# Optimization experiments

Hardware: AMD Instinct MI355X
Metric: run time of the kernel (lower is better)

The kernel has to match this reference:

```python
import jax, jax.numpy as jnp
import numpy as np

C_S = 128
C_T = 128
C_OUT = 128


def _proj(x, W, b):
    # 1x1x1 Conv3d == per-voxel linear over channel dim. x: [B, Cin, T, H, W]
    return jnp.einsum('oc,bcthw->bothw', W, x) + b[None, :, None, None, None]


def setup_inputs() -> dict:
    key = jax.random.key(0)
    ks = jax.random.split(key, 12)
    B, T, H, W = 4, 4, 32, 32
    spatial_features = jax.random.normal(ks[0], (B, T, C_S, H, W), dtype=jnp.float32)
    temporal_features = jax.random.normal(ks[1], (B, C_T, T, H, W), dtype=jnp.float32)
    def w(k, o, i):
        return jax.random.normal(k, (o, i), dtype=jnp.float32) * (i ** -0.5)
    return {
        'spatial_features': spatial_features,
        'temporal_features': temporal_features,
        'Wq': w(ks[2], C_OUT, C_S), 'bq': jnp.zeros((C_OUT,), jnp.float32),
        'Wk': w(ks[3], C_OUT, C_T), 'bk': jnp.zeros((C_OUT,), jnp.float32),
        'Wv': w(ks[4], C_OUT, C_T), 'bv': jnp.zeros((C_OUT,), jnp.float32),
        'Wo': w(ks[5], C_OUT, C_OUT), 'bo': jnp.zeros((C_OUT,), jnp.float32),
    }


def reference(spatial_features, temporal_features, Wq, bq, Wk, bk, Wv, bv, Wo, bo):
    B, T, C_s, H, W = spatial_features.shape
    N = T * H * W
    scale = C_OUT ** -0.5
    # permute(0,2,1,3,4): [B, T, C_s, H, W] -> [B, C_s, T, H, W]
    x_s = jnp.transpose(spatial_features, (0, 2, 1, 3, 4))
    q = _proj(x_s, Wq, bq)                 # [B, C_out, T, H, W]
    k = _proj(temporal_features, Wk, bk)   # [B, C_out, T, H, W]
    v = _proj(temporal_features, Wv, bv)   # [B, C_out, T, H, W]
    Q = q.reshape(B, C_OUT, N).transpose(0, 2, 1)  # [B, N, C]
    K = k.reshape(B, C_OUT, N)                     # [B, C, N]
    V = v.reshape(B, C_OUT, N).transpose(0, 2, 1)  # [B, N, C]
    attn = jax.nn.softmax(jnp.einsum('bnc,bcm->bnm', Q, K) * scale, axis=2)  # [B, N, N]
    out = jnp.einsum('bnm,bmc->bnc', attn, V)      # [B, N, C]
    out = out.transpose(0, 2, 1).reshape(B, C_OUT, T, H, W)
    return _proj(out, Wo, bo)
```

## Files before the change

### kernel.cpp

```cpp
#include <hip/hip_runtime.h>
#include <cstddef>

#define NDIM 4096
#define SCALE 0.08838834764831843f
#define SOFT_BIAS 8.0f

typedef _Float16 h8 __attribute__((ext_vector_type(8)));
typedef _Float16 h4 __attribute__((ext_vector_type(4)));
typedef _Float16 h2 __attribute__((ext_vector_type(2)));
typedef float    f4 __attribute__((ext_vector_type(4)));

__global__ __launch_bounds__(256) void prep_w_kernel(
    const float* __restrict__ Wq, const float* __restrict__ Wk,
    const float* __restrict__ Wv, const float* __restrict__ Wo,
    _Float16* __restrict__ Wh)
{
    const int idx = (blockIdx.x * 256 + threadIdx.x) * 8;
    const int sel = idx >> 14;
    const float* src = sel == 0 ? Wq : sel == 1 ? Wk : sel == 2 ? Wv : Wo;
    const int off = idx & 16383;
    const float4 a = *(const float4*)(src + off);
    const float4 c = *(const float4*)(src + off + 4);
    h8 r;
    r[0]=(_Float16)a.x; r[1]=(_Float16)a.y; r[2]=(_Float16)a.z; r[3]=(_Float16)a.w;
    r[4]=(_Float16)c.x; r[5]=(_Float16)c.y; r[6]=(_Float16)c.z; r[7]=(_Float16)c.w;
    *(h8*)(Wh + idx) = r;
}

__global__ __launch_bounds__(64) void proj_q_kernel(
    const float* __restrict__ spatial, const _Float16* __restrict__ Whq,
    const float* __restrict__ bq, _Float16* __restrict__ Qh)
{
    __shared__ __align__(16) _Float16 Xl[16 * 136];
    const int lane = threadIdx.x;
    const int n0   = blockIdx.x * 16;
    const int b    = blockIdx.y;
    const int t    = n0 >> 10, hw0 = n0 & 1023;
    const int n16  = lane & 15, q4 = lane >> 4;

    {
        const float* sb = spatial + (((size_t)(b * 4 + t) * 128 + q4 * 32) << 10) + hw0 + n16;
        #pragma unroll
        for (int cp = 0; cp < 16; ++cp) {
            const float v0 = sb[(size_t)(2 * cp) << 10];
            const float v1 = sb[(size_t)(2 * cp + 1) << 10];
            h2 pk; pk[0] = (_Float16)v0; pk[1] = (_Float16)v1;
            *(h2*)&Xl[n16 * 136 + q4 * 32 + 2 * cp] = pk;
        }
    }
    __builtin_amdgcn_wave_barrier();

    h8 xf[4];
    #pragma unroll
    for (int ks = 0; ks < 4; ++ks)
        xf[ks] = *(const h8*)&Xl[n16 * 136 + 32 * ks + 8 * q4];

    f4 acc[8];
    #pragma unroll
    for (int ot = 0; ot < 8; ++ot) acc[ot] = (f4)0.0f;

    #pragma unroll
    for (int ot = 0; ot < 8; ++ot)
        #pragma unroll
        for (int ks = 0; ks < 4; ++ks) {
            const h8 af = *(const h8*)(Whq + (16 * ot + n16) * 128 + 32 * ks + 8 * q4);
            acc[ot] = __builtin_amdgcn_mfma_f32_16x16x32_f16(af, xf[ks], acc[ot], 0, 0, 0);
        }

    #pragma unroll
    for (int ot = 0; ot < 8; ++ot) {
        const float4 bb = *(const float4*)&bq[16 * ot + 4 * q4];
        h4 r;
        r[0]=(_Float16)(acc[ot][0]+bb.x); r[1]=(_Float16)(acc[ot][1]+bb.y);
        r[2]=(_Float16)(acc[ot][2]+bb.z); r[3]=(_Float16)(acc[ot][3]+bb.w);
        *(h4*)(Qh + ((size_t)b * NDIM + n0 + n16) * 128 + 16 * ot + 4 * q4) = r;
    }
}

__global__ __launch_bounds__(64) void proj_kv_kernel(
    const float* __restrict__ temporal, const _Float16* __restrict__ Whk,
    const _Float16* __restrict__ Whv, const float* __restrict__ bk,
    const float* __restrict__ bv, _Float16* __restrict__ Kh, _Float16* __restrict__ Vt)
{
    __shared__ __align__(16) _Float16 Xl[16 * 136];
    const int lane = threadIdx.x;
    const int n0   = blockIdx.x * 16;
    const int b    = blockIdx.y;
    const int n16  = lane & 15, q4 = lane >> 4;

    {
        const float* sb = temporal + (((size_t)(b * 128 + q4 * 32)) << 12) + n0 + n16;
        #pragma unroll
        for (int cp = 0; cp < 16; ++cp) {
            const float v0 = sb[(size_t)(2 * cp) << 12];
            const float v1 = sb[(size_t)(2 * cp + 1) << 12];
            h2 pk; pk[0] = (_Float16)v0; pk[1] = (_Float16)v1;
            *(h2*)&Xl[n16 * 136 + q4 * 32 + 2 * cp] = pk;
        }
    }
    __builtin_amdgcn_wave_barrier();

    h8 xf[4];
    #pragma unroll
    for (int ks = 0; ks < 4; ++ks)
        xf[ks] = *(const h8*)&Xl[n16 * 136 + 32 * ks + 8 * q4];

    f4 accK[8], accV[8];
    #pragma unroll
    for (int i = 0; i < 8; ++i) { accK[i] = (f4)0.0f; accV[i] = (f4)0.0f; }

    #pragma unroll
    for (int ot = 0; ot < 8; ++ot)
        #pragma unroll
        for (int ks = 0; ks < 4; ++ks) {
            const h8 af = *(const h8*)(Whk + (16 * ot + n16) * 128 + 32 * ks + 8 * q4);
            accK[ot] = __builtin_amdgcn_mfma_f32_16x16x32_f16(af, xf[ks], accK[ot], 0, 0, 0);
        }
    #pragma unroll
    for (int ct = 0; ct < 8; ++ct)
        #pragma unroll
        for (int ks = 0; ks < 4; ++ks) {
            const h8 bf = *(const h8*)(Whv + (16 * ct + n16) * 128 + 32 * ks + 8 * q4);
            accV[ct] = __builtin_amdgcn_mfma_f32_16x16x32_f16(xf[ks], bf, accV[ct], 0, 0, 0);
        }

    #pragma unroll
    for (int ot = 0; ot < 8; ++ot) {
        const float4 bb = *(const float4*)&bk[16 * ot + 4 * q4];
        h4 r;
        r[0]=(_Float16)(accK[ot][0]+bb.x); r[1]=(_Float16)(accK[ot][1]+bb.y);
        r[2]=(_Float16)(accK[ot][2]+bb.z); r[3]=(_Float16)(accK[ot][3]+bb.w);
        *(h4*)(Kh + ((size_t)b * NDIM + n0 + n16) * 128 + 16 * ot + 4 * q4) = r;
    }
    #pragma unroll
    for (int ct = 0; ct < 8; ++ct) {
        const float bb = bv[16 * ct + n16];
        h4 r;
        r[0]=(_Float16)(accV[ct][0]+bb); r[1]=(_Float16)(accV[ct][1]+bb);
        r[2]=(_Float16)(accV[ct][2]+bb); r[3]=(_Float16)(accV[ct][3]+bb);
        *(h4*)(Vt + ((size_t)(b * 128 + 16 * ct + n16) << 12) + n0 + 4 * q4) = r;
    }
}

__global__ __launch_bounds__(512, 2) void attn_kernel(
    const _Float16* __restrict__ Qh, const _Float16* __restrict__ Kh,
    const _Float16* __restrict__ Vt, _Float16* __restrict__ Opart,
    float* __restrict__ lpart)
{
    __shared__ __align__(16) _Float16 sh[19712];
    _Float16* __restrict__ Kt = sh;
    _Float16* __restrict__ Vl = sh + 4352;
    _Float16* __restrict__ Pa = sh + 9472;

    const int tid  = threadIdx.x;
    const int w    = tid >> 6, lane = tid & 63;
    const int g    = w >> 1,  p    = w & 1;
    const int n16  = lane & 15, q4 = lane >> 4;
    const int b    = blockIdx.z, hf = blockIdx.y;
    const int n0   = blockIdx.x * 256;
    const int mb   = hf * 1024;

    _Float16* __restrict__ Pg = Pa + g * (64 * 40);

    h8 qf[2][4];
    {
        const _Float16* Qb = Qh + ((size_t)b * NDIM + n0 + 64 * g + 32 * p + n16) * 128;
        #pragma unroll
        for (int qs = 0; qs < 2; ++qs)
            #pragma unroll
            for (int ks = 0; ks < 4; ++ks)
                qf[qs][ks] = *(const h8*)(Qb + (size_t)(16 * qs) * 128 + 32 * ks + 8 * q4);
    }

    const int km  = tid >> 4, kc8 = (tid & 15) * 8;
    const int vc  = tid >> 2, vm8 = (tid & 3) * 8;
    const _Float16* kp = Kh + ((size_t)b * NDIM + mb + km) * 128 + kc8;
    const _Float16* vp = Vt + (((size_t)(b * 128 + vc)) << 12) + mb + vm8;
    int4 kreg = *(const int4*)kp;
    int4 vreg = *(const int4*)vp;

    f4 oacc[4][4];
    #pragma unroll
    for (int i = 0; i < 4; ++i)
        #pragma unroll
        for (int j = 0; j < 4; ++j) oacc[i][j] = (f4)0.0f;
    float lsum[2] = {0.0f, 0.0f};

    for (int it = 0; it < 32; ++it) {
        __syncthreads();
        *(int4*)&Kt[km * 136 + kc8] = kreg;
        *(int4*)&Vl[vc * 40  + vm8] = vreg;
        __syncthreads();

        if (it < 31) {
            kp += 32 * 128; vp += 32;
            kreg = *(const int4*)kp;
            vreg = *(const int4*)vp;
        }

        f4 sacc[2][2];
        #pragma unroll
        for (int mt = 0; mt < 2; ++mt) { sacc[mt][0] = (f4)0.0f; sacc[mt][1] = (f4)0.0f; }
        #pragma unroll
        for (int mt = 0; mt < 2; ++mt)
            #pragma unroll
            for (int ks = 0; ks < 4; ++ks) {
                const h8 kf = *(const h8*)&Kt[(16 * mt + n16) * 136 + 32 * ks + 8 * q4];
                sacc[mt][0] = __builtin_amdgcn_mfma_f32_16x16x32_f16(kf, qf[0][ks], sacc[mt][0], 0, 0, 0);
                sacc[mt][1] = __builtin_amdgcn_mfma_f32_16x16x32_f16(kf, qf[1][ks], sacc[mt][1], 0, 0, 0);
            }

        #pragma unroll
        for (int mt = 0; mt < 2; ++mt)
            #pragma unroll
            for (int qs = 0; qs < 2; ++qs) {
                h4 pk;
                #pragma unroll
                for (int r = 0; r < 4; ++r) {
                    const float e = __expf(fmaf(sacc[mt][qs][r], SCALE, -SOFT_BIAS));
                    lsum[qs] += e;
                    pk[r] = (_Float16)e;
                }
                *(h4*)&Pg[(32 * p + 16 * qs + n16) * 40 + 16 * mt + 4 * q4] = pk;
            }
        __syncthreads();

        h8 pf[4], vf[4];
        #pragma unroll
        for (int qs4 = 0; qs4 < 4; ++qs4)
            pf[qs4] = *(const h8*)&Pg[(16 * qs4 + n16) * 40 + 8 * q4];
        #pragma unroll
        for (int ct = 0; ct < 4; ++ct)
            vf[ct] = *(const h8*)&Vl[(64 * p + 16 * ct + n16) * 40 + 8 * q4];
        #pragma unroll
        for (int qs4 = 0; qs4 < 4; ++qs4)
            #pragma unroll
            for (int ct = 0; ct < 4; ++ct)
                oacc[qs4][ct] = __builtin_amdgcn_mfma_f32_16x16x32_f16(pf[qs4], vf[ct], oacc[qs4][ct], 0, 0, 0);
    }

    #pragma unroll
    for (int qs = 0; qs < 2; ++qs) {
        lsum[qs] += __shfl_xor(lsum[qs], 16, 64);
        lsum[qs] += __shfl_xor(lsum[qs], 32, 64);
    }
    if (lane < 16) {
        float* lb = lpart + (size_t)(hf * 4 + b) * NDIM + n0 + 64 * g + 32 * p;
        lb[lane]      = lsum[0];
        lb[16 + lane] = lsum[1];
    }

    for (int g2 = 0; g2 < 4; ++g2) {
        __syncthreads();
        if (g == g2) {
            #pragma unroll
            for (int qs4 = 0; qs4 < 4; ++qs4)
                #pragma unroll
                for (int ct = 0; ct < 4; ++ct)
                    #pragma unroll
                    for (int r = 0; r < 4; ++r)
                        sh[(16 * qs4 + 4 * q4 + r) * 136 + 64 * p + 16 * ct + n16] =
                            (_Float16)oacc[qs4][ct][r];
        }
        __syncthreads();
        const size_t ob = ((size_t)(hf * 4 + b) * NDIM + n0 + 64 * g2) * 128;
        #pragma unroll
        for (int i = 0; i < 2; ++i) {
            const int ii  = tid + 512 * i;
            const int row = ii >> 4, c8 = (ii & 15) * 8;
            *(int4*)(Opart + ob + (size_t)row * 128 + c8) = *(const int4*)&sh[row * 136 + c8];
        }
    }
}

__global__ __launch_bounds__(64) void proj_final_kernel(
    const _Float16* __restrict__ Opart, const float* __restrict__ lpart,
    const _Float16* __restrict__ Who, const float* __restrict__ bo,
    float* __restrict__ out)
{
    __shared__ __align__(16) _Float16 Xl[16 * 136];
    const int lane = threadIdx.x;
    const int n0   = blockIdx.x * 16;
    const int b    = blockIdx.y;
    const int n16  = lane & 15, q4 = lane >> 4;

    #pragma unroll
    for (int i = 0; i < 4; ++i) {
        const int ii  = lane + 64 * i;
        const int row = ii >> 4, c8 = (ii & 15) * 8;
        float vals[8] = {0,0,0,0,0,0,0,0};
        float l = 0.0f;
        #pragma unroll
        for (int hf = 0; hf < 4; ++hf) {
            const size_t base = ((size_t)(hf * 4 + b) * NDIM + n0 + row) * 128 + c8;
            const h8 o = *(const h8*)(Opart + base);
            #pragma unroll
            for (int j = 0; j < 8; ++j) vals[j] += (float)o[j];
            l += lpart[(size_t)(hf * 4 + b) * NDIM + n0 + row];
        }
        const float rinv = 1.0f / l;
        h8 r;
        #pragma unroll
        for (int j = 0; j < 8; ++j) r[j] = (_Float16)(vals[j] * rinv);
        *(h8*)&Xl[row * 136 + c8] = r;
    }
    __builtin_amdgcn_wave_barrier();

    h8 xf[4];
    #pragma unroll
    for (int ks = 0; ks < 4; ++ks)
        xf[ks] = *(const h8*)&Xl[n16 * 136 + 32 * ks + 8 * q4];

    f4 acc[8];
    #pragma unroll
    for (int ot = 0; ot < 8; ++ot) acc[ot] = (f4)0.0f;

    #pragma unroll
    for (int ot = 0; ot < 8; ++ot)
        #pragma unroll
        for (int ks = 0; ks < 4; ++ks) {
            const h8 af = *(const h8*)(Who + (16 * ot + n16) * 128 + 32 * ks + 8 * q4);
            acc[ot] = __builtin_amdgcn_mfma_f32_16x16x32_f16(af, xf[ks], acc[ot], 0, 0, 0);
        }

    #pragma unroll
    for (int ot = 0; ot < 8; ++ot) {
        const float4 bb = *(const float4*)&bo[16 * ot + 4 * q4];
        const float bias[4] = {bb.x, bb.y, bb.z, bb.w};
        #pragma unroll
        for (int r = 0; r < 4; ++r)
            out[((size_t)(b * 128 + 16 * ot + 4 * q4 + r) << 12) + n0 + n16] =
                acc[ot][r] + bias[r];
    }
}

extern "C" void kernel_launch(void* const* d_in, const int* in_sizes, int n_in,
                              void* d_out, int out_size, void* d_ws, size_t ws_size,
                              hipStream_t stream)
{
    const float* spatial  = (const float*)d_in[0];
    const float* temporal = (const float*)d_in[1];
    const float* Wq = (const float*)d_in[2];
    const float* bq = (const float*)d_in[3];
    const float* Wk = (const float*)d_in[4];
    const float* bk = (const float*)d_in[5];
    const float* Wv = (const float*)d_in[6];
    const float* bv = (const float*)d_in[7];
    const float* Wo = (const float*)d_in[8];
    const float* bo = (const float*)d_in[9];

    char* ws = (char*)d_ws;
    _Float16* Qh    = (_Float16*)(ws);
    _Float16* Kh    = (_Float16*)(ws + (4u  << 20));
    _Float16* Vt    = (_Float16*)(ws + (8u  << 20));
    _Float16* Opart = (_Float16*)(ws + (12u << 20));
    float*    lpart = (float*)   (ws + (28u << 20));
    _Float16* Wh    = (_Float16*)(ws + (28u << 20) + (256u << 10));

    prep_w_kernel<<<32, 256, 0, stream>>>(Wq, Wk, Wv, Wo, Wh);
    proj_q_kernel<<<dim3(256, 4), 64, 0, stream>>>(spatial, Wh, bq, Qh);
    proj_kv_kernel<<<dim3(256, 4), 64, 0, stream>>>(temporal, Wh + 16384, Wh + 32768,
                                                    bk, bv, Kh, Vt);
    attn_kernel<<<dim3(16, 4, 4), 512, 0, stream>>>(Qh, Kh, Vt, Opart, lpart);
    proj_final_kernel<<<dim3(256, 4), 64, 0, stream>>>(Opart, lpart, Wh + 49152, bo,
                                                       (float*)d_out);
}
```

Measured before the change: 157.9 us.

## Fuse Q/K/V projections, retile attention to 256 threads, coalesce I/O

```diff
diff --git a/kernel.cpp b/kernel.cpp
--- a/kernel.cpp
+++ b/kernel.cpp
@@ -27,127 +27,125 @@
     *(h8*)(Wh + idx) = r;
 }
 
-__global__ __launch_bounds__(64) void proj_q_kernel(
-    const float* __restrict__ spatial, const _Float16* __restrict__ Whq,
-    const float* __restrict__ bq, _Float16* __restrict__ Qh)
+__global__ __launch_bounds__(256, 1) void proj_qkv_kernel(
+    const float* __restrict__ spatial, const float* __restrict__ temporal,
+    const _Float16* __restrict__ Wh,
+    const float* __restrict__ bq, const float* __restrict__ bk,
+    const float* __restrict__ bv,
+    _Float16* __restrict__ Qh, _Float16* __restrict__ Kh, _Float16* __restrict__ Vt)
 {
-    __shared__ __align__(16) _Float16 Xl[16 * 136];
-    const int lane = threadIdx.x;
-    const int n0   = blockIdx.x * 16;
-    const int b    = blockIdx.y;
-    const int t    = n0 >> 10, hw0 = n0 & 1023;
-    const int n16  = lane & 15, q4 = lane >> 4;
+    __shared__ __align__(16) _Float16 Xs[64 * 152];
+    __shared__ __align__(16) _Float16 Xt[64 * 152];
+    const int tid = threadIdx.x;
+    const int n0  = blockIdx.x * 64;
+    const int b   = blockIdx.y;
+    const int t   = n0 >> 10, hw0 = n0 & 1023;
+
+    #pragma unroll
+    for (int i = 0; i < 8; ++i) {
+        const int ii = tid + 256 * i;
+        const int c = ii >> 4, j = ii & 15;
+        const float4 v = *(const float4*)(spatial + (((size_t)(b * 4 + t) * 128 + c) << 10)
+                                          + hw0 + 4 * j);
+        Xs[(4 * j + 0) * 152 + c] = (_Float16)v.x;
+        Xs[(4 * j + 1) * 152 + c] = (_Float16)v.y;
+        Xs[(4 * j + 2) * 152 + c] = (_Float16)v.z;
+        Xs[(4 * j + 3) * 152 + c] = (_Float16)v.w;
+    }
+    #pragma unroll
+    for (int i = 0; i < 8; ++i) {
+        const int ii = tid + 256 * i;
+        const int c = ii >> 4, j = ii & 15;
+        const float4 v = *(const float4*)(temporal + (((size_t)(b * 128 + c)) << 12)
+                                          + n0 + 4 * j);
+        Xt[(4 * j + 0) * 152 + c] = (_Float16)v.x;
+        Xt[(4 * j + 1) * 152 + c] = (_Float16)v.y;
+        Xt[(4 * j + 2) * 152 + c] = (_Float16)v.z;
+        Xt[(4 * j + 3) * 152 + c] = (_Float16)v.w;
+    }
+    __syncthreads();
+
+    const int w = tid >> 6, n16 = tid & 15, q4 = (tid >> 4) & 3;
+    const _Float16* __restrict__ Whq = Wh;
+    const _Float16* __restrict__ Whk = Wh + 16384;
+    const _Float16* __restrict__ Whv = Wh + 32768;
+
+    h8 xs_f[4], xt_f[4];
+    #pragma unroll
+    for (int ks = 0; ks < 4; ++ks) {
+        xs_f[ks] = *(const h8*)&Xs[(16 * w + n16) * 152 + 32 * ks + 8 * q4];
+        xt_f[ks] = *(const h8*)&Xt[(16 * w + n16) * 152 + 32 * ks + 8 * q4];
+    }
 
     {
-        const float* sb = spatial + (((size_t)(b * 4 + t) * 128 + q4 * 32) << 10) + hw0 + n16;
-        #pragma unroll
-        for (int cp = 0; cp < 16; ++cp) {
-            const float v0 = sb[(size_t)(2 * cp) << 10];
-            const float v1 = sb[(size_t)(2 * cp + 1) << 10];
-            h2 pk; pk[0] = (_Float16)v0; pk[1] = (_Float16)v1;
-            *(h2*)&Xl[n16 * 136 + q4 * 32 + 2 * cp] = pk;
-        }
-    }
-    __builtin_amdgcn_wave_barrier();
-
-    h8 xf[4];
-    #pragma unroll
-    for (int ks = 0; ks < 4; ++ks)
-        xf[ks] = *(const h8*)&Xl[n16 * 136 + 32 * ks + 8 * q4];
-
-    f4 acc[8];
-    #pragma unroll
-    for (int ot = 0; ot < 8; ++ot) acc[ot] = (f4)0.0f;
-
-    #pragma unroll
-    for (int ot = 0; ot < 8; ++ot)
-        #pragma unroll
-        for (int ks = 0; ks < 4; ++ks) {
-            const h8 af = *(const h8*)(Whq + (16 * ot + n16) * 128 + 32 * ks + 8 * q4);
-            acc[ot] = __builtin_amdgcn_mfma_f32_16x16x32_f16(af, xf[ks], acc[ot], 0, 0, 0);
-        }
-
-    #pragma unroll
-    for (int ot = 0; ot < 8; ++ot) {
-        const float4 bb = *(const float4*)&bq[16 * ot + 4 * q4];
-        h4 r;
-        r[0]=(_Float16)(acc[ot][0]+bb.x); r[1]=(_Float16)(acc[ot][1]+bb.y);
-        r[2]=(_Float16)(acc[ot][2]+bb.z); r[3]=(_Float16)(acc[ot][3]+bb.w);
-        *(h4*)(Qh + ((size_t)b * NDIM + n0 + n16) * 128 + 16 * ot + 4 * q4) = r;
+        f4 acc[8];
+        #pragma unroll
+        for (int ot = 0; ot < 8; ++ot) acc[ot] = (f4)0.0f;
+        #pragma unroll
+        for (int ot = 0; ot < 8; ++ot)
+            #pragma unroll
+            for (int ks = 0; ks < 4; ++ks) {
+                const h8 af = *(const h8*)(Whq + (16 * ot + n16) * 128 + 32 * ks + 8 * q4);
+                acc[ot] = __builtin_amdgcn_mfma_f32_16x16x32_f16(af, xs_f[ks], acc[ot], 0, 0, 0);
+            }
+        #pragma unroll
+        for (int ot = 0; ot < 8; ++ot) {
+            const float4 bb = *(const float4*)&bq[16 * ot + 4 * q4];
+            h4 r;
+            r[0]=(_Float16)(acc[ot][0]+bb.x); r[1]=(_Float16)(acc[ot][1]+bb.y);
+            r[2]=(_Float16)(acc[ot][2]+bb.z); r[3]=(_Float16)(acc[ot][3]+bb.w);
+            *(h4*)(Qh + ((size_t)b * NDIM + n0 + 16 * w + n16) * 128 + 16 * ot + 4 * q4) = r;
+        }
+    }
+    {
+        f4 acc[8];
+        #pragma unroll
+        for (int ot = 0; ot < 8; ++ot) acc[ot] = (f4)0.0f;
+        #pragma unroll
+        for (int ot = 0; ot < 8; ++ot)
+            #pragma unroll
+            for (int ks = 0; ks < 4; ++ks) {
+                const h8 af = *(const h8*)(Whk + (16 * ot + n16) * 128 + 32 * ks + 8 * q4);
+                acc[ot] = __builtin_amdgcn_mfma_f32_16x16x32_f16(af, xt_f[ks], acc[ot], 0, 0, 0);
+            }
+        #pragma unroll
+        for (int ot = 0; ot < 8; ++ot) {
+            const float4 bb = *(const float4*)&bk[16 * ot + 4 * q4];
+            h4 r;
+            r[0]=(_Float16)(acc[ot][0]+bb.x); r[1]=(_Float16)(acc[ot][1]+bb.y);
+            r[2]=(_Float16)(acc[ot][2]+bb.z); r[3]=(_Float16)(acc[ot][3]+bb.w);
+            *(h4*)(Kh + ((size_t)b * NDIM + n0 + 16 * w + n16) * 128 + 16 * ot + 4 * q4) = r;
+        }
+    }
+    {
+        f4 acc[8];
+        #pragma unroll
+        for (int ct = 0; ct < 8; ++ct) acc[ct] = (f4)0.0f;
+        #pragma unroll
+        for (int ct = 0; ct < 8; ++ct)
+            #pragma unroll
+            for (int ks = 0; ks < 4; ++ks) {
+                const h8 bf = *(const h8*)(Whv + (16 * ct + n16) * 128 + 32 * ks + 8 * q4);
+                acc[ct] = __builtin_amdgcn_mfma_f32_16x16x32_f16(xt_f[ks], bf, acc[ct], 0, 0, 0);
+            }
+        #pragma unroll
+        for (int ct = 0; ct < 8; ++ct) {
+            const float bb = bv[16 * ct + n16];
+            h4 r;
+            r[0]=(_Float16)(acc[ct][0]+bb); r[1]=(_Float16)(acc[ct][1]+bb);
+            r[2]=(_Float16)(acc[ct][2]+bb); r[3]=(_Float16)(acc[ct][3]+bb);
+            *(h4*)(Vt + ((size_t)(b * 128 + 16 * ct + n16) << 12) + n0 + 16 * w + 4 * q4) = r;
+        }
     }
 }
 
-__global__ __launch_bounds__(64) void proj_kv_kernel(
-    const float* __restrict__ temporal, const _Float16* __restrict__ Whk,
-    const _Float16* __restrict__ Whv, const float* __restrict__ bk,
-    const float* __restrict__ bv, _Float16* __restrict__ Kh, _Float16* __restrict__ Vt)
-{
-    __shared__ __align__(16) _Float16 Xl[16 * 136];
-    const int lane = threadIdx.x;
-    const int n0   = blockIdx.x * 16;
-    const int b    = blockIdx.y;
-    const int n16  = lane & 15, q4 = lane >> 4;
-
-    {
-        const float* sb = temporal + (((size_t)(b * 128 + q4 * 32)) << 12) + n0 + n16;
-        #pragma unroll
-        for (int cp = 0; cp < 16; ++cp) {
-            const float v0 = sb[(size_t)(2 * cp) << 12];
-            const float v1 = sb[(size_t)(2 * cp + 1) << 12];
-            h2 pk; pk[0] = (_Float16)v0; pk[1] = (_Float16)v1;
-            *(h2*)&Xl[n16 * 136 + q4 * 32 + 2 * cp] = pk;
-        }
-    }
-    __builtin_amdgcn_wave_barrier();
-
-    h8 xf[4];
-    #pragma unroll
-    for (int ks = 0; ks < 4; ++ks)
-        xf[ks] = *(const h8*)&Xl[n16 * 136 + 32 * ks + 8 * q4];
-
-    f4 accK[8], accV[8];
-    #pragma unroll
-    for (int i = 0; i < 8; ++i) { accK[i] = (f4)0.0f; accV[i] = (f4)0.0f; }
-
-    #pragma unroll
-    for (int ot = 0; ot < 8; ++ot)
-        #pragma unroll
-        for (int ks = 0; ks < 4; ++ks) {
-            const h8 af = *(const h8*)(Whk + (16 * ot + n16) * 128 + 32 * ks + 8 * q4);
-            accK[ot] = __builtin_amdgcn_mfma_f32_16x16x32_f16(af, xf[ks], accK[ot], 0, 0, 0);
-        }
-    #pragma unroll
-    for (int ct = 0; ct < 8; ++ct)
-        #pragma unroll
-        for (int ks = 0; ks < 4; ++ks) {
-            const h8 bf = *(const h8*)(Whv + (16 * ct + n16) * 128 + 32 * ks + 8 * q4);
-            accV[ct] = __builtin_amdgcn_mfma_f32_16x16x32_f16(xf[ks], bf, accV[ct], 0, 0, 0);
-        }
-
-    #pragma unroll
-    for (int ot = 0; ot < 8; ++ot) {
-        const float4 bb = *(const float4*)&bk[16 * ot + 4 * q4];
-        h4 r;
-        r[0]=(_Float16)(accK[ot][0]+bb.x); r[1]=(_Float16)(accK[ot][1]+bb.y);
-        r[2]=(_Float16)(accK[ot][2]+bb.z); r[3]=(_Float16)(accK[ot][3]+bb.w);
-        *(h4*)(Kh + ((size_t)b * NDIM + n0 + n16) * 128 + 16 * ot + 4 * q4) = r;
-    }
-    #pragma unroll
-    for (int ct = 0; ct < 8; ++ct) {
-        const float bb = bv[16 * ct + n16];
-        h4 r;
-        r[0]=(_Float16)(accV[ct][0]+bb); r[1]=(_Float16)(accV[ct][1]+bb);
-        r[2]=(_Float16)(accV[ct][2]+bb); r[3]=(_Float16)(accV[ct][3]+bb);
-        *(h4*)(Vt + ((size_t)(b * 128 + 16 * ct + n16) << 12) + n0 + 4 * q4) = r;
-    }
-}
-
-__global__ __launch_bounds__(512, 2) void attn_kernel(
+__global__ __launch_bounds__(256, 2) void attn_kernel(
     const _Float16* __restrict__ Qh, const _Float16* __restrict__ Kh,
     const _Float16* __restrict__ Vt, _Float16* __restrict__ Opart,
     float* __restrict__ lpart)
 {
-    __shared__ __align__(16) _Float16 sh[19712];
+    __shared__ __align__(16) _Float16 sh[14592];
+    __shared__ float lred[2][2][32];
     _Float16* __restrict__ Kt = sh;
     _Float16* __restrict__ Vl = sh + 4352;
     _Float16* __restrict__ Pa = sh + 9472;
@@ -157,16 +155,16 @@
     const int g    = w >> 1,  p    = w & 1;
     const int n16  = lane & 15, q4 = lane >> 4;
     const int b    = blockIdx.z, hf = blockIdx.y;
-    const int n0   = blockIdx.x * 256;
+    const int n0   = blockIdx.x * 128;
     const int mb   = hf * 1024;
 
     _Float16* __restrict__ Pg = Pa + g * (64 * 40);
 
-    h8 qf[2][4];
+    h8 qf[4][4];
     {
-        const _Float16* Qb = Qh + ((size_t)b * NDIM + n0 + 64 * g + 32 * p + n16) * 128;
-        #pragma unroll
-        for (int qs = 0; qs < 2; ++qs)
+        const _Float16* Qb = Qh + ((size_t)b * NDIM + n0 + 64 * g + n16) * 128;
+        #pragma unroll
+        for (int qs = 0; qs < 4; ++qs)
             #pragma unroll
             for (int ks = 0; ks < 4; ++ks)
                 qf[qs][ks] = *(const h8*)(Qb + (size_t)(16 * qs) * 128 + 32 * ks + 8 * q4);
@@ -176,117 +174,146 @@
     const int vc  = tid >> 2, vm8 = (tid & 3) * 8;
     const _Float16* kp = Kh + ((size_t)b * NDIM + mb + km) * 128 + kc8;
     const _Float16* vp = Vt + (((size_t)(b * 128 + vc)) << 12) + mb + vm8;
-    int4 kreg = *(const int4*)kp;
-    int4 vreg = *(const int4*)vp;
+    int4 kreg0 = *(const int4*)kp;
+    int4 kreg1 = *(const int4*)(kp + (size_t)16 * 128);
+    int4 vreg0 = *(const int4*)vp;
+    int4 vreg1 = *(const int4*)(vp + ((size_t)64 << 12));
 
     f4 oacc[4][4];
     #pragma unroll
     for (int i = 0; i < 4; ++i)
         #pragma unroll
         for (int j = 0; j < 4; ++j) oacc[i][j] = (f4)0.0f;
-    float lsum[2] = {0.0f, 0.0f};
+    float lsum[4] = {0.0f, 0.0f, 0.0f, 0.0f};
 
     for (int it = 0; it < 32; ++it) {
         __syncthreads();
-        *(int4*)&Kt[km * 136 + kc8] = kreg;
-        *(int4*)&Vl[vc * 40  + vm8] = vreg;
+        *(int4*)&Kt[km * 136 + kc8]        = kreg0;
+        *(int4*)&Kt[(16 + km) * 136 + kc8] = kreg1;
+        *(int4*)&Vl[vc * 40 + vm8]         = vreg0;
+        *(int4*)&Vl[(64 + vc) * 40 + vm8]  = vreg1;
         __syncthreads();
 
         if (it < 31) {
             kp += 32 * 128; vp += 32;
-            kreg = *(const int4*)kp;
-            vreg = *(const int4*)vp;
-        }
-
-        f4 sacc[2][2];
-        #pragma unroll
-        for (int mt = 0; mt < 2; ++mt) { sacc[mt][0] = (f4)0.0f; sacc[mt][1] = (f4)0.0f; }
-        #pragma unroll
-        for (int mt = 0; mt < 2; ++mt)
-            #pragma unroll
-            for (int ks = 0; ks < 4; ++ks) {
-                const h8 kf = *(const h8*)&Kt[(16 * mt + n16) * 136 + 32 * ks + 8 * q4];
-                sacc[mt][0] = __builtin_amdgcn_mfma_f32_16x16x32_f16(kf, qf[0][ks], sacc[mt][0], 0, 0, 0);
-                sacc[mt][1] = __builtin_amdgcn_mfma_f32_16x16x32_f16(kf, qf[1][ks], sacc[mt][1], 0, 0, 0);
+            kreg0 = *(const int4*)kp;
+            kreg1 = *(const int4*)(kp + (size_t)16 * 128);
+            vreg0 = *(const int4*)vp;
+            vreg1 = *(const int4*)(vp + ((size_t)64 << 12));
+        }
+
+        f4 sacc[4];
+        #pragma unroll
+        for (int qs = 0; qs < 4; ++qs) sacc[qs] = (f4)0.0f;
+        #pragma unroll
+        for (int ks = 0; ks < 4; ++ks) {
+            const h8 kf = *(const h8*)&Kt[(16 * p + n16) * 136 + 32 * ks + 8 * q4];
+            #pragma unroll
+            for (int qs = 0; qs < 4; ++qs)
+                sacc[qs] = __builtin_amdgcn_mfma_f32_16x16x32_f16(kf, qf[qs][ks], sacc[qs], 0, 0, 0);
+        }
+
+        #pragma unroll
+        for (int qs = 0; qs < 4; ++qs) {
+            h4 pk;
+            #pragma unroll
+            for (int r = 0; r < 4; ++r) {
+                const float e = __expf(fmaf(sacc[qs][r], SCALE, -SOFT_BIAS));
+                lsum[qs] += e;
+                pk[r] = (_Float16)e;
             }
-
-        #pragma unroll
-        for (int mt = 0; mt < 2; ++mt)
-            #pragma unroll
-            for (int qs = 0; qs < 2; ++qs) {
-                h4 pk;
-                #pragma unroll
-                for (int r = 0; r < 4; ++r) {
-                    const float e = __expf(fmaf(sacc[mt][qs][r], SCALE, -SOFT_BIAS));
-                    lsum[qs] += e;
-                    pk[r] = (_Float16)e;
-                }
-                *(h4*)&Pg[(32 * p + 16 * qs + n16) * 40 + 16 * mt + 4 * q4] = pk;
-            }
+            *(h4*)&Pg[(16 * qs + n16) * 40 + 16 * p + 4 * q4] = pk;
+        }
         __syncthreads();
 
         h8 pf[4], vf[4];
         #pragma unroll
-        for (int qs4 = 0; qs4 < 4; ++qs4)
-            pf[qs4] = *(const h8*)&Pg[(16 * qs4 + n16) * 40 + 8 * q4];
+        for (int qs = 0; qs < 4; ++qs)
+            pf[qs] = *(const h8*)&Pg[(16 * qs + n16) * 40 + 8 * q4];
         #pragma unroll
         for (int ct = 0; ct < 4; ++ct)
             vf[ct] = *(const h8*)&Vl[(64 * p + 16 * ct + n16) * 40 + 8 * q4];
         #pragma unroll
-        for (int qs4 = 0; qs4 < 4; ++qs4)
+        for (int qs = 0; qs < 4; ++qs)
             #pragma unroll
             for (int ct = 0; ct < 4; ++ct)
-                oacc[qs4][ct] = __builtin_amdgcn_mfma_f32_16x16x32_f16(pf[qs4], vf[ct], oacc[qs4][ct], 0, 0, 0);
-    }
-
-    #pragma unroll
-    for (int qs = 0; qs < 2; ++qs) {
+                oacc[qs][ct] = __builtin_amdgcn_mfma_f32_16x16x32_f16(pf[qs], vf[ct], oacc[qs][ct], 0, 0, 0);
+    }
+
+    #pragma unroll
+    for (int qs = 0; qs < 4; ++qs) {
         lsum[qs] += __shfl_xor(lsum[qs], 16, 64);
         lsum[qs] += __shfl_xor(lsum[qs], 32, 64);
     }
-    if (lane < 16) {
-        float* lb = lpart + (size_t)(hf * 4 + b) * NDIM + n0 + 64 * g + 32 * p;
-        lb[lane]      = lsum[0];
-        lb[16 + lane] = lsum[1];
-    }
-
-    for (int g2 = 0; g2 < 4; ++g2) {
+    __syncthreads();
+    if (q4 == 0) {
+        #pragma unroll
+        for (int qs = 0; qs < 4; ++qs) lred[g][p][0] = lred[g][p][0];
+        #pragma unroll
+        for (int qs = 0; qs < 2; ++qs) {
+            lred[g][p][16 * qs + n16]      = lsum[qs];
+        }
+    }
+    __syncthreads();
+    if (q4 == 0) {
+        float* lb = lpart + (size_t)(hf * 4 + b) * NDIM + n0 + 64 * g;
+        if (p == 0) {
+            #pragma unroll
+            for (int qs = 0; qs < 2; ++qs)
+                lb[16 * qs + n16] = lred[g][0][16 * qs + n16] + lred[g][1][16 * qs + n16];
+        }
+    }
+    __syncthreads();
+    if (q4 == 0) {
+        #pragma unroll
+        for (int qs = 2; qs < 4; ++qs)
+            lred[g][p][16 * (qs - 2) + n16] = lsum[qs];
+    }
+    __syncthreads();
+    if (q4 == 0 && p == 0) {
+        float* lb = lpart + (size_t)(hf * 4 + b) * NDIM + n0 + 64 * g + 32;
+        #pragma unroll
+        for (int qs = 0; qs < 2; ++qs)
+            lb[16 * qs + n16] = lred[g][0][16 * qs + n16] + lred[g][1][16 * qs + n16];
+    }
+
+    for (int g2 = 0; g2 < 2; ++g2) {
         __syncthreads();
         if (g == g2) {
             #pragma unroll
-            for (int qs4 = 0; qs4 < 4; ++qs4)
+            for (int qs = 0; qs < 4; ++qs)
                 #pragma unroll
                 for (int ct = 0; ct < 4; ++ct)
                     #pragma unroll
                     for (int r = 0; r < 4; ++r)
-                        sh[(16 * qs4 + 4 * q4 + r) * 136 + 64 * p + 16 * ct + n16] =
-                            (_Float16)oacc[qs4][ct][r];
+                        sh[(16 * qs + 4 * q4 + r) * 136 + 64 * p + 16 * ct + n16] =
+                            (_Float16)oacc[qs][ct][r];
         }
         __syncthreads();
         const size_t ob = ((size_t)(hf * 4 + b) * NDIM + n0 + 64 * g2) * 128;
         #pragma unroll
-        for (int i = 0; i < 2; ++i) {
-            const int ii  = tid + 512 * i;
+        for (int i = 0; i < 4; ++i) {
+            const int ii  = tid + 256 * i;
             const int row = ii >> 4, c8 = (ii & 15) * 8;
             *(int4*)(Opart + ob + (size_t)row * 128 + c8) = *(const int4*)&sh[row * 136 + c8];
         }
     }
 }
 
-__global__ __launch_bounds__(64) void proj_final_kernel(
+__global__ __launch_bounds__(256, 1) void proj_final_kernel(
     const _Float16* __restrict__ Opart, const float* __restrict__ lpart,
     const _Float16* __restrict__ Who, const float* __restrict__ bo,
     float* __restrict__ out)
 {
-    __shared__ __align__(16) _Float16 Xl[16 * 136];
-    const int lane = threadIdx.x;
-    const int n0   = blockIdx.x * 16;
-    const int b    = blockIdx.y;
-    const int n16  = lane & 15, q4 = lane >> 4;
+    __shared__ __align__(16) _Float16 Xl[64 * 136];
+    __shared__ __align__(16) float Ofin[128 * 68];
+    const int tid = threadIdx.x;
+    const int n0  = blockIdx.x * 64;
+    const int b   = blockIdx.y;
 
     #pragma unroll
     for (int i = 0; i < 4; ++i) {
-        const int ii  = lane + 64 * i;
+        const int ii  = tid + 256 * i;
         const int row = ii >> 4, c8 = (ii & 15) * 8;
         float vals[8] = {0,0,0,0,0,0,0,0};
         float l = 0.0f;
@@ -304,12 +331,14 @@
         for (int j = 0; j < 8; ++j) r[j] = (_Float16)(vals[j] * rinv);
         *(h8*)&Xl[row * 136 + c8] = r;
     }
-    __builtin_amdgcn_wave_barrier();
+    __syncthreads();
+
+    const int w = tid >> 6, n16 = tid & 15, q4 = (tid >> 4) & 3;
 
     h8 xf[4];
     #pragma unroll
     for (int ks = 0; ks < 4; ++ks)
-        xf[ks] = *(const h8*)&Xl[n16 * 136 + 32 * ks + 8 * q4];
+        xf[ks] = *(const h8*)&Xl[(16 * w + n16) * 136 + 32 * ks + 8 * q4];
 
     f4 acc[8];
     #pragma unroll
@@ -329,8 +358,15 @@
         const float bias[4] = {bb.x, bb.y, bb.z, bb.w};
         #pragma unroll
         for (int r = 0; r < 4; ++r)
-            out[((size_t)(b * 128 + 16 * ot + 4 * q4 + r) << 12) + n0 + n16] =
-                acc[ot][r] + bias[r];
+            Ofin[(16 * ot + 4 * q4 + r) * 68 + 16 * w + n16] = acc[ot][r] + bias[r];
+    }
+    __syncthreads();
+    #pragma unroll
+    for (int i = 0; i < 8; ++i) {
+        const int ii  = tid + 256 * i;
+        const int row = ii >> 4, j = ii & 15;
+        *(float4*)(out + (((size_t)(b * 128 + row)) << 12) + n0 + 4 * j) =
+            *(const float4*)&Ofin[row * 68 + 4 * j];
     }
 }
 
@@ -358,10 +394,9 @@
     _Float16* Wh    = (_Float16*)(ws + (28u << 20) + (256u << 10));
 
     prep_w_kernel<<<32, 256, 0, stream>>>(Wq, Wk, Wv, Wo, Wh);
-    proj_q_kernel<<<dim3(256, 4), 64, 0, stream>>>(spatial, Wh, bq, Qh);
-    proj_kv_kernel<<<dim3(256, 4), 64, 0, stream>>>(temporal, Wh + 16384, Wh + 32768,
-                                                    bk, bv, Kh, Vt);
-    attn_kernel<<<dim3(16, 4, 4), 512, 0, stream>>>(Qh, Kh, Vt, Opart, lpart);
-    proj_final_kernel<<<dim3(256, 4), 64, 0, stream>>>(Opart, lpart, Wh + 49152, bo,
+    proj_qkv_kernel<<<dim3(64, 4), 256, 0, stream>>>(spatial, temporal, Wh,
+                                                     bq, bk, bv, Qh, Kh, Vt);
+    attn_kernel<<<dim3(32, 4, 4), 256, 0, stream>>>(Qh, Kh, Vt, Opart, lpart);
+    proj_final_kernel<<<dim3(64, 4), 256, 0, stream>>>(Opart, lpart, Wh + 49152, bo,
                                                        (float*)d_out);
 }
```

Result: slower. 164.0 us (+3.9%).
